# Kernel optimization log

Hardware: AMD Instinct MI355X
Metric: run time of the kernel (lower is better)

Reference implementation:

```python
import jax, jax.numpy as jnp
import numpy as np

N = 50000      # nodes
E = 200000     # edges
IN = 768       # in_dim
HID = 256      # hidden_dim
OUT = 64       # out_dim
H = 4          # heads in conv1
R = 6          # n_relations
NEG = 0.2      # LeakyReLU negative slope (PyG default)
EPS = 1e-5     # LayerNorm eps


def layer_norm(h, g, b):
    mu = jnp.mean(h, axis=-1, keepdims=True)
    var = jnp.mean((h - mu) ** 2, axis=-1, keepdims=True)
    return (h - mu) * jax.lax.rsqrt(var + EPS) * g + b


def gat_layer(x, src, dst, W, a_src, a_dst, bias, heads, dh):
    # project: [N, heads, dh]
    h = (x @ W).reshape(-1, heads, dh)
    # per-node attention logits [N, heads]
    al_s = jnp.sum(h * a_src, axis=-1)
    al_d = jnp.sum(h * a_dst, axis=-1)
    # per-edge scores (edge j->i: source contributes al_s[j], target al_d[i])
    e = jax.nn.leaky_relu(al_s[src] + al_d[dst], NEG)  # [E, heads]
    # segment softmax over edges sharing the same destination node
    e_max = jax.ops.segment_max(e, dst, num_segments=N)        # [N, heads]
    ex = jnp.exp(e - e_max[dst])                               # [E, heads]
    denom = jax.ops.segment_sum(ex, dst, num_segments=N)       # [N, heads]
    alpha = ex / denom[dst]                                    # [E, heads]
    # weighted scatter-aggregate of source messages
    msg = h[src] * alpha[:, :, None]                            # [E, heads, dh]
    out = jax.ops.segment_sum(msg, dst, num_segments=N)        # [N, heads, dh]
    return out.reshape(-1, heads * dh) + bias


def setup_inputs() -> dict:
    key = jax.random.key(0)
    ks = jax.random.split(key, 16)
    s = 0.05  # keep attention logits tame
    return {
        "x": jax.random.normal(ks[0], (N, IN), jnp.float32),
        "edge_index": jax.random.randint(ks[1], (2, E), 0, N, dtype=jnp.int64),
        "edge_type": jax.random.randint(ks[2], (E,), 0, R, dtype=jnp.int64),
        "edge_emb": jax.random.normal(ks[3], (R, IN), jnp.float32) * s,
        "W1": jax.random.normal(ks[4], (IN, H * (HID // H)), jnp.float32) * s,
        "a_src1": jax.random.normal(ks[5], (H, HID // H), jnp.float32) * s,
        "a_dst1": jax.random.normal(ks[6], (H, HID // H), jnp.float32) * s,
        "b1": jnp.zeros((HID,), jnp.float32),
        "g1": jnp.ones((HID,), jnp.float32),
        "be1": jnp.zeros((HID,), jnp.float32),
        "W2": jax.random.normal(ks[7], (HID, OUT), jnp.float32) * s,
        "a_src2": jax.random.normal(ks[8], (1, OUT), jnp.float32) * s,
        "a_dst2": jax.random.normal(ks[9], (1, OUT), jnp.float32) * s,
        "b2": jnp.zeros((OUT,), jnp.float32),
        "g2": jnp.ones((OUT,), jnp.float32),
        "be2": jnp.zeros((OUT,), jnp.float32),
    }


def reference(x, edge_index, edge_type, edge_emb, W1, a_src1, a_dst1, b1, g1, be1,
              W2, a_src2, a_dst2, b2, g2, be2):
    src, dst = edge_index[0], edge_index[1]
    edge_feat = edge_emb[edge_type]                 # [E, IN]
    x_mod = x.at[src].set(x[src] + edge_feat)
    h = gat_layer(x_mod, src, dst, W1, a_src1, a_dst1, b1, H, HID // H)
    h = layer_norm(h, g1, be1)
    h = jax.nn.elu(h)                                # dropout off (inference)
    h = gat_layer(h, src, dst, W2, a_src2, a_dst2, b2, 1, OUT)
    h = layer_norm(h, g2, be2)
    return h
```

## Files before the change

### kernel.cpp

```cpp
#include <hip/hip_runtime.h>
#include <cstdint>
#include <cstddef>

#define NN 50000
#define NE 200000
#define IND 768
#define HID 256
#define OUTD 64
#define NB 196

typedef __bf16 bf16;
typedef __bf16 bf16x8 __attribute__((ext_vector_type(8)));
typedef float f32x4 __attribute__((ext_vector_type(4)));

__device__ __forceinline__ void ld_lds16(const void* g, void* l) {
  __builtin_amdgcn_global_load_lds((const __attribute__((address_space(1))) void*)g,
                                   (__attribute__((address_space(3))) void*)l, 16, 0, 0);
}

__global__ __launch_bounds__(256) void k_edge_prep(const int* __restrict__ ei,
                                                   int* __restrict__ le, int* __restrict__ deg) {
  int e = blockIdx.x * 256 + threadIdx.x;
  if (e < NE) {
    atomicMax(&le[ei[e]], e);
    atomicAdd(&deg[ei[NE + e]], 1);
  }
}

__global__ __launch_bounds__(256) void k_scan_block(const int* __restrict__ deg,
                                                    int* __restrict__ excl, int* __restrict__ bsum) {
  __shared__ int sm[256];
  int tid = threadIdx.x;
  int i = blockIdx.x * 256 + tid;
  int v = (i < NN) ? deg[i] : 0;
  sm[tid] = v;
  __syncthreads();
#pragma unroll
  for (int off = 1; off < 256; off <<= 1) {
    int t = (tid >= off) ? sm[tid - off] : 0;
    __syncthreads();
    sm[tid] += t;
    __syncthreads();
  }
  if (i < NN) excl[i] = sm[tid] - v;
  if (tid == 255) bsum[blockIdx.x] = sm[255];
}

__global__ __launch_bounds__(256) void k_scan_partials(const int* __restrict__ bsum,
                                                       int* __restrict__ bbase) {
  __shared__ int sm[256];
  int tid = threadIdx.x;
  int v = (tid < NB) ? bsum[tid] : 0;
  sm[tid] = v;
  __syncthreads();
#pragma unroll
  for (int off = 1; off < 256; off <<= 1) {
    int t = (tid >= off) ? sm[tid - off] : 0;
    __syncthreads();
    sm[tid] += t;
    __syncthreads();
  }
  bbase[tid] = sm[tid] - v;
}

__global__ __launch_bounds__(256) void k_add_base(const int* __restrict__ excl,
                                                  const int* __restrict__ bbase,
                                                  const int* __restrict__ le,
                                                  const int* __restrict__ et,
                                                  int* __restrict__ rowstart, int* __restrict__ cur,
                                                  int* __restrict__ tmod) {
  int i = blockIdx.x * 256 + threadIdx.x;
  if (i < NN) {
    int rs = excl[i] + bbase[i >> 8];
    rowstart[i] = rs;
    cur[i] = rs;
    int l = le[i];
    tmod[i] = (l >= 0) ? et[l] : -1;
  }
}

__global__ __launch_bounds__(256) void k_scatter_csr(const int* __restrict__ ei,
                                                     int* __restrict__ cur, int* __restrict__ csr) {
  int e = blockIdx.x * 256 + threadIdx.x;
  if (e < NE) {
    int d = ei[NE + e];
    int pos = atomicAdd(&cur[d], 1);
    csr[pos] = ei[e];
  }
}

__global__ __launch_bounds__(256) void k_prep(const float* __restrict__ W1,
                                              const float* __restrict__ W2,
                                              const float* __restrict__ eemb,
                                              bf16* __restrict__ W1t,
                                              bf16* __restrict__ W2t,
                                              float* __restrict__ P) {
  int b = blockIdx.x, tid = threadIdx.x;
  if (b < 768) {
    int k = b, n = tid;
    W1t[n * 768 + k] = (bf16)W1[k * 256 + n];
  } else if (b < 768 + 64) {
    int k = (b - 768) * 4 + (tid >> 6);
    int n = tid & 63;
    W2t[n * 256 + k] = (bf16)W2[k * 64 + n];
  } else {
    int r = b - 832, c = tid;
    float s = 0.f;
    for (int k = 0; k < 768; k++) s += eemb[r * 768 + k] * W1[k * 256 + c];
    P[r * 256 + c] = s;
  }
}

__global__ __launch_bounds__(256) void k_gemm1(const float* __restrict__ Ax,
                                               const bf16* __restrict__ Bt,
                                               const int* __restrict__ tmod,
                                               const float* __restrict__ P,
                                               bf16* __restrict__ C,
                                               const float* __restrict__ aS,
                                               const float* __restrict__ aD,
                                               float* __restrict__ alS,
                                               float* __restrict__ alD) {
  __shared__ float As[128 * 32];
  __shared__ bf16 Bs[128 * 32];
  const int tid = threadIdx.x, lane = tid & 63, wave = tid >> 6;
  const int wr = wave >> 1, wc = wave & 1;
  const int ln15 = lane & 15, q = lane >> 4;
  const int n0 = blockIdx.x * 128, m0 = blockIdx.y * 128;

  const int a_lrow = lane >> 3, a_gch = (lane & 7) ^ a_lrow;
  const int b_lrow = lane >> 2, b_gch = (lane & 3) ^ ((b_lrow >> 1) & 3);

  f32x4 acc[4][4] = {};

  for (int kt = 0; kt < IND; kt += 32) {
    __syncthreads();
#pragma unroll
    for (int j = 0; j < 4; j++) {
      int g = wave * 4 + j;
      int grow = min(m0 + g * 8 + a_lrow, NN - 1);
      ld_lds16(Ax + (size_t)grow * IND + kt + a_gch * 4, As + g * 256);
    }
#pragma unroll
    for (int j = 0; j < 2; j++) {
      int h = wave * 2 + j;
      int grow = h * 16 + b_lrow;
      ld_lds16(Bt + (size_t)(n0 + grow) * IND + kt + b_gch * 8, Bs + h * 512);
    }
    __syncthreads();

    bf16x8 af[4], bfr[4];
    const float4* Asv = (const float4*)As;
#pragma unroll
    for (int mi = 0; mi < 4; mi++) {
      int R = wr * 64 + mi * 16 + ln15, msk = R & 7;
      float4 f0 = Asv[R * 8 + ((2 * q) ^ msk)];
      float4 f1 = Asv[R * 8 + ((2 * q + 1) ^ msk)];
      bf16x8 t;
      t[0] = (bf16)f0.x; t[1] = (bf16)f0.y; t[2] = (bf16)f0.z; t[3] = (bf16)f0.w;
      t[4] = (bf16)f1.x; t[5] = (bf16)f1.y; t[6] = (bf16)f1.z; t[7] = (bf16)f1.w;
      af[mi] = t;
    }
#pragma unroll
    for (int ni = 0; ni < 4; ni++) {
      int R = wc * 64 + ni * 16 + ln15;
      int c = q ^ ((R >> 1) & 3);
      bfr[ni] = *(const bf16x8*)(Bs + R * 32 + c * 8);
    }
#pragma unroll
    for (int mi = 0; mi < 4; mi++)
#pragma unroll
      for (int ni = 0; ni < 4; ni++)
        acc[mi][ni] = __builtin_amdgcn_mfma_f32_16x16x32_bf16(af[mi], bfr[ni], acc[mi][ni], 0, 0, 0);
  }

  const int hd = (n0 + wc * 64) >> 6;
#pragma unroll
  for (int mi = 0; mi < 4; mi++) {
#pragma unroll
    for (int r = 0; r < 4; r++) {
      int row = m0 + wr * 64 + mi * 16 + q * 4 + r;
      bool vr = row < NN;
      int t = tmod[vr ? row : NN - 1];
      float ps = 0.f, pd = 0.f;
#pragma unroll
      for (int ni = 0; ni < 4; ni++) {
        int col = n0 + wc * 64 + ni * 16 + ln15;
        float val = acc[mi][ni][r];
        if (t >= 0) val += P[t * HID + col];
        ps += val * aS[col];
        pd += val * aD[col];
        if (vr) C[(size_t)row * HID + col] = (bf16)val;
      }
#pragma unroll
      for (int o = 1; o < 16; o <<= 1) { ps += __shfl_xor(ps, o); pd += __shfl_xor(pd, o); }
      if (ln15 == 0 && vr) { alS[row * 4 + hd] = ps; alD[row * 4 + hd] = pd; }
    }
  }
}

__global__ __launch_bounds__(256) void k_gemm2(const bf16* __restrict__ A,
                                               const bf16* __restrict__ Bt,
                                               float* __restrict__ C,
                                               const float* __restrict__ aS,
                                               const float* __restrict__ aD,
                                               float* __restrict__ alS,
                                               float* __restrict__ alD) {
  __shared__ bf16 As[128 * 32];
  __shared__ bf16 Bs[64 * 32];
  const int tid = threadIdx.x, lane = tid & 63, wave = tid >> 6;
  const int ln15 = lane & 15, q = lane >> 4;
  const int m0 = blockIdx.x * 128;
  const int b_lrow = lane >> 2, b_gch = (lane & 3) ^ ((b_lrow >> 1) & 3);

  f32x4 acc[2][4] = {};

  for (int kt = 0; kt < HID; kt += 32) {
    __syncthreads();
#pragma unroll
    for (int j = 0; j < 2; j++) {
      int h = wave * 2 + j;
      int grow = min(m0 + h * 16 + b_lrow, NN - 1);
      ld_lds16(A + (size_t)grow * HID + kt + b_gch * 8, As + h * 512);
    }
    {
      int grow = wave * 16 + b_lrow;
      ld_lds16(Bt + (size_t)grow * HID + kt + b_gch * 8, Bs + wave * 512);
    }
    __syncthreads();

    bf16x8 af[2], bfr[4];
#pragma unroll
    for (int mi = 0; mi < 2; mi++) {
      int R = wave * 32 + mi * 16 + ln15;
      int c = q ^ ((R >> 1) & 3);
      af[mi] = *(const bf16x8*)(As + R * 32 + c * 8);
    }
#pragma unroll
    for (int ni = 0; ni < 4; ni++) {
      int R = ni * 16 + ln15;
      int c = q ^ ((R >> 1) & 3);
      bfr[ni] = *(const bf16x8*)(Bs + R * 32 + c * 8);
    }
#pragma unroll
    for (int mi = 0; mi < 2; mi++)
#pragma unroll
      for (int ni = 0; ni < 4; ni++)
        acc[mi][ni] = __builtin_amdgcn_mfma_f32_16x16x32_bf16(af[mi], bfr[ni], acc[mi][ni], 0, 0, 0);
  }

#pragma unroll
  for (int mi = 0; mi < 2; mi++) {
#pragma unroll
    for (int r = 0; r < 4; r++) {
      int row = m0 + wave * 32 + mi * 16 + q * 4 + r;
      bool vr = row < NN;
      float ps = 0.f, pd = 0.f;
#pragma unroll
      for (int ni = 0; ni < 4; ni++) {
        int col = ni * 16 + ln15;
        float val = acc[mi][ni][r];
        ps += val * aS[col];
        pd += val * aD[col];
        if (vr) C[(size_t)row * OUTD + col] = val;
      }
#pragma unroll
      for (int o = 1; o < 16; o <<= 1) { ps += __shfl_xor(ps, o); pd += __shfl_xor(pd, o); }
      if (ln15 == 0 && vr) { alS[row] = ps; alD[row] = pd; }
    }
  }
}

__global__ __launch_bounds__(256) void k_agg_ln1(const int* __restrict__ rowstart,
                                                 const int* __restrict__ deg,
                                                 const int* __restrict__ csr,
                                                 const bf16* __restrict__ h1,
                                                 const float* __restrict__ alS,
                                                 const float* __restrict__ alD,
                                                 const float* __restrict__ b1,
                                                 const float* __restrict__ g1,
                                                 const float* __restrict__ be1,
                                                 bf16* __restrict__ hln) {
  __shared__ float red[8];
  int n = blockIdx.x, f = threadIdx.x, hd = f >> 6;
  int start = rowstart[n], cnt = deg[n];
  float ald = alD[n * 4 + hd];
  float accv = 0.f, accw = 0.f;
  for (int j0 = 0; j0 < cnt; j0 += 8) {
    int m = cnt - j0; m = m > 8 ? 8 : m;
    int sj[8]; float wv[8];
#pragma unroll
    for (int jj = 0; jj < 8; jj++) sj[jj] = (jj < m) ? csr[start + j0 + jj] : 0;
#pragma unroll
    for (int jj = 0; jj < 8; jj++) {
      float lg = alS[sj[jj] * 4 + hd] + ald;
      lg = lg >= 0.f ? lg : 0.2f * lg;
      wv[jj] = (jj < m) ? __expf(lg) : 0.f;
    }
#pragma unroll
    for (int jj = 0; jj < 8; jj++) {
      accv += wv[jj] * (float)h1[(size_t)sj[jj] * HID + f];
      accw += wv[jj];
    }
  }
  float v = (cnt > 0) ? accv / accw : 0.f;
  v += b1[f];
  float s = v, ss = v * v;
#pragma unroll
  for (int off = 32; off; off >>= 1) { s += __shfl_xor(s, off); ss += __shfl_xor(ss, off); }
  if ((f & 63) == 0) { red[f >> 6] = s; red[4 + (f >> 6)] = ss; }
  __syncthreads();
  float tot = red[0] + red[1] + red[2] + red[3];
  float tss = red[4] + red[5] + red[6] + red[7];
  float mu = tot * (1.f / HID);
  float var = tss * (1.f / HID) - mu * mu;
  float y = (v - mu) * rsqrtf(var + 1e-5f) * g1[f] + be1[f];
  y = y > 0.f ? y : __expf(y) - 1.f;
  hln[(size_t)n * HID + f] = (bf16)y;
}

__global__ __launch_bounds__(256) void k_agg_ln2(const int* __restrict__ rowstart,
                                                 const int* __restrict__ deg,
                                                 const int* __restrict__ csr,
                                                 const float* __restrict__ h2,
                                                 const float* __restrict__ alS,
                                                 const float* __restrict__ alD,
                                                 const float* __restrict__ b2,
                                                 const float* __restrict__ g2,
                                                 const float* __restrict__ be2,
                                                 float* __restrict__ out) {
  int n = blockIdx.x * 4 + (threadIdx.x >> 6);
  int f = threadIdx.x & 63;
  int start = rowstart[n], cnt = deg[n];
  float ald = alD[n];
  float accv = 0.f, accw = 0.f;
  for (int j0 = 0; j0 < cnt; j0 += 8) {
    int m = cnt - j0; m = m > 8 ? 8 : m;
    int sj[8]; float wv[8];
#pragma unroll
    for (int jj = 0; jj < 8; jj++) sj[jj] = (jj < m) ? csr[start + j0 + jj] : 0;
#pragma unroll
    for (int jj = 0; jj < 8; jj++) {
      float lg = alS[sj[jj]] + ald;
      lg = lg >= 0.f ? lg : 0.2f * lg;
      wv[jj] = (jj < m) ? __expf(lg) : 0.f;
    }
#pragma unroll
    for (int jj = 0; jj < 8; jj++) {
      accv += wv[jj] * h2[(size_t)sj[jj] * OUTD + f];
      accw += wv[jj];
    }
  }
  float v = (cnt > 0) ? accv / accw : 0.f;
  v += b2[f];
  float s = v, ss = v * v;
#pragma unroll
  for (int off = 32; off; off >>= 1) { s += __shfl_xor(s, off); ss += __shfl_xor(ss, off); }
  float mu = s * (1.f / OUTD);
  float var = ss * (1.f / OUTD) - mu * mu;
  out[(size_t)n * OUTD + f] = (v - mu) * rsqrtf(var + 1e-5f) * g2[f] + be2[f];
}

extern "C" void kernel_launch(void* const* d_in, const int* in_sizes, int n_in,
                              void* d_out, int out_size, void* d_ws, size_t ws_size,
                              hipStream_t stream) {
  const float* x    = (const float*)d_in[0];
  const int*   ei   = (const int*)d_in[1];
  const int*   et   = (const int*)d_in[2];
  const float* eemb = (const float*)d_in[3];
  const float* W1   = (const float*)d_in[4];
  const float* as1  = (const float*)d_in[5];
  const float* ad1  = (const float*)d_in[6];
  const float* b1   = (const float*)d_in[7];
  const float* g1   = (const float*)d_in[8];
  const float* be1  = (const float*)d_in[9];
  const float* W2   = (const float*)d_in[10];
  const float* as2  = (const float*)d_in[11];
  const float* ad2  = (const float*)d_in[12];
  const float* b2   = (const float*)d_in[13];
  const float* g2   = (const float*)d_in[14];
  const float* be2  = (const float*)d_in[15];
  float* out = (float*)d_out;

  char* base = (char*)d_ws;
  size_t off = 0;
  auto alloc = [&](size_t bytes) -> void* {
    void* p = base + off;
    off = (off + bytes + 255) & ~(size_t)255;
    return p;
  };
  int*   le    = (int*)alloc((size_t)NN * 4);
  int*   deg   = (int*)alloc((size_t)NN * 4);
  int*   excl  = (int*)alloc((size_t)NN * 4);
  int*   bsum  = (int*)alloc(256 * 4);
  int*   bbase = (int*)alloc(256 * 4);
  int*   rowst = (int*)alloc((size_t)NN * 4);
  int*   cur   = (int*)alloc((size_t)NN * 4);
  int*   tmod  = (int*)alloc((size_t)NN * 4);
  int*   csr   = (int*)alloc((size_t)NE * 4);
  bf16*  h1    = (bf16*)alloc((size_t)NN * HID * 2);
  float* alS1  = (float*)alloc((size_t)NN * 4 * 4);
  float* alD1  = (float*)alloc((size_t)NN * 4 * 4);
  bf16*  hln   = (bf16*)alloc((size_t)NN * HID * 2);
  float* h2    = (float*)alloc((size_t)NN * OUTD * 4);
  float* alS2  = (float*)alloc((size_t)NN * 4);
  float* alD2  = (float*)alloc((size_t)NN * 4);
  bf16*  W1t   = (bf16*)alloc((size_t)HID * IND * 2);
  bf16*  W2t   = (bf16*)alloc((size_t)OUTD * HID * 2);
  float* P     = (float*)alloc(6 * HID * 4);

  hipMemsetAsync(le, 0xFF, (size_t)NN * 4, stream);
  hipMemsetAsync(deg, 0, (size_t)NN * 4, stream);

  k_edge_prep<<<(NE + 255) / 256, 256, 0, stream>>>(ei, le, deg);
  k_scan_block<<<NB, 256, 0, stream>>>(deg, excl, bsum);
  k_scan_partials<<<1, 256, 0, stream>>>(bsum, bbase);
  k_add_base<<<NB, 256, 0, stream>>>(excl, bbase, le, et, rowst, cur, tmod);
  k_scatter_csr<<<(NE + 255) / 256, 256, 0, stream>>>(ei, cur, csr);

  k_prep<<<838, 256, 0, stream>>>(W1, W2, eemb, W1t, W2t, P);

  k_gemm1<<<dim3(2, (NN + 127) / 128), 256, 0, stream>>>(x, W1t, tmod, P, h1, as1, ad1, alS1, alD1);
  k_agg_ln1<<<NN, 256, 0, stream>>>(rowst, deg, csr, h1, alS1, alD1, b1, g1, be1, hln);

  k_gemm2<<<(NN + 127) / 128, 256, 0, stream>>>(hln, W2t, h2, as2, ad2, alS2, alD2);
  k_agg_ln2<<<NN / 4, 256, 0, stream>>>(rowst, deg, csr, h2, alS2, alD2, b2, g2, be2, out);
}
```

Before: 518.4 us.

## Double-buffer GEMM tiles via registers and simplify aggregation loops

Both GEMM kernels move from direct global-to-LDS async loads with a single buffer to register-staged double buffering. The next K tile is prefetched into registers while MFMAs run on the current LDS buffer, which removes one barrier per iteration. GEMM1 now converts the fp32 A operand to bf16 before the LDS store, halving A's LDS footprint, and XOR swizzles are replaced by 40-element padded rows. The aggregation kernels drop the batched 8-wide gather for a simple per-edge loop, which loses memory-level parallelism on the gathers.

```diff
diff --git a/kernel.cpp b/kernel.cpp
--- a/kernel.cpp
+++ b/kernel.cpp
@@ -10,13 +10,9 @@
 #define NB 196
 
 typedef __bf16 bf16;
+typedef __bf16 bf16x4 __attribute__((ext_vector_type(4)));
 typedef __bf16 bf16x8 __attribute__((ext_vector_type(8)));
 typedef float f32x4 __attribute__((ext_vector_type(4)));
-
-__device__ __forceinline__ void ld_lds16(const void* g, void* l) {
-  __builtin_amdgcn_global_load_lds((const __attribute__((address_space(1))) void*)g,
-                                   (__attribute__((address_space(3))) void*)l, 16, 0, 0);
-}
 
 __global__ __launch_bounds__(256) void k_edge_prep(const int* __restrict__ ei,
                                                    int* __restrict__ le, int* __restrict__ deg) {
@@ -120,57 +116,64 @@
                                                const float* __restrict__ aD,
                                                float* __restrict__ alS,
                                                float* __restrict__ alD) {
-  __shared__ float As[128 * 32];
-  __shared__ bf16 Bs[128 * 32];
+  __shared__ bf16 As[2][128 * 40];
+  __shared__ bf16 Bs[2][128 * 40];
   const int tid = threadIdx.x, lane = tid & 63, wave = tid >> 6;
   const int wr = wave >> 1, wc = wave & 1;
   const int ln15 = lane & 15, q = lane >> 4;
   const int n0 = blockIdx.x * 128, m0 = blockIdx.y * 128;
 
-  const int a_lrow = lane >> 3, a_gch = (lane & 7) ^ a_lrow;
-  const int b_lrow = lane >> 2, b_gch = (lane & 3) ^ ((b_lrow >> 1) & 3);
+  const int ar = tid >> 3, ac = (tid & 7) * 4;
+  const int br = tid >> 2, bc = (tid & 3) * 8;
+
+  int arow[4];
+#pragma unroll
+  for (int j = 0; j < 4; j++) arow[j] = min(m0 + j * 32 + ar, NN - 1);
+
+  float4 rA[4];
+  int4 rB[2];
+  auto loadT = [&](int kt) {
+#pragma unroll
+    for (int j = 0; j < 4; j++)
+      rA[j] = *(const float4*)(Ax + (size_t)arow[j] * IND + kt + ac);
+#pragma unroll
+    for (int j = 0; j < 2; j++)
+      rB[j] = *(const int4*)(Bt + (size_t)(n0 + j * 64 + br) * IND + kt + bc);
+  };
+  auto storeT = [&](int p) {
+#pragma unroll
+    for (int j = 0; j < 4; j++) {
+      bf16x4 t;
+      t[0] = (bf16)rA[j].x; t[1] = (bf16)rA[j].y; t[2] = (bf16)rA[j].z; t[3] = (bf16)rA[j].w;
+      *(bf16x4*)(&As[p][(j * 32 + ar) * 40 + ac]) = t;
+    }
+#pragma unroll
+    for (int j = 0; j < 2; j++)
+      *(int4*)(&Bs[p][(j * 64 + br) * 40 + bc]) = rB[j];
+  };
 
   f32x4 acc[4][4] = {};
-
+  loadT(0);
+  storeT(0);
+  int p = 0;
   for (int kt = 0; kt < IND; kt += 32) {
     __syncthreads();
-#pragma unroll
-    for (int j = 0; j < 4; j++) {
-      int g = wave * 4 + j;
-      int grow = min(m0 + g * 8 + a_lrow, NN - 1);
-      ld_lds16(Ax + (size_t)grow * IND + kt + a_gch * 4, As + g * 256);
-    }
-#pragma unroll
-    for (int j = 0; j < 2; j++) {
-      int h = wave * 2 + j;
-      int grow = h * 16 + b_lrow;
-      ld_lds16(Bt + (size_t)(n0 + grow) * IND + kt + b_gch * 8, Bs + h * 512);
-    }
-    __syncthreads();
-
+    bool more = (kt + 32) < IND;
+    if (more) loadT(kt + 32);
     bf16x8 af[4], bfr[4];
-    const float4* Asv = (const float4*)As;
-#pragma unroll
-    for (int mi = 0; mi < 4; mi++) {
-      int R = wr * 64 + mi * 16 + ln15, msk = R & 7;
-      float4 f0 = Asv[R * 8 + ((2 * q) ^ msk)];
-      float4 f1 = Asv[R * 8 + ((2 * q + 1) ^ msk)];
-      bf16x8 t;
-      t[0] = (bf16)f0.x; t[1] = (bf16)f0.y; t[2] = (bf16)f0.z; t[3] = (bf16)f0.w;
-      t[4] = (bf16)f1.x; t[5] = (bf16)f1.y; t[6] = (bf16)f1.z; t[7] = (bf16)f1.w;
-      af[mi] = t;
-    }
-#pragma unroll
-    for (int ni = 0; ni < 4; ni++) {
-      int R = wc * 64 + ni * 16 + ln15;
-      int c = q ^ ((R >> 1) & 3);
-      bfr[ni] = *(const bf16x8*)(Bs + R * 32 + c * 8);
-    }
+#pragma unroll
+    for (int mi = 0; mi < 4; mi++)
+      af[mi] = *(const bf16x8*)(&As[p][(wr * 64 + mi * 16 + ln15) * 40 + q * 8]);
+#pragma unroll
+    for (int ni = 0; ni < 4; ni++)
+      bfr[ni] = *(const bf16x8*)(&Bs[p][(wc * 64 + ni * 16 + ln15) * 40 + q * 8]);
 #pragma unroll
     for (int mi = 0; mi < 4; mi++)
 #pragma unroll
       for (int ni = 0; ni < 4; ni++)
         acc[mi][ni] = __builtin_amdgcn_mfma_f32_16x16x32_bf16(af[mi], bfr[ni], acc[mi][ni], 0, 0, 0);
+    if (more) storeT(p ^ 1);
+    p ^= 1;
   }
 
   const int hd = (n0 + wc * 64) >> 6;
@@ -205,47 +208,53 @@
                                                const float* __restrict__ aD,
                                                float* __restrict__ alS,
                                                float* __restrict__ alD) {
-  __shared__ bf16 As[128 * 32];
-  __shared__ bf16 Bs[64 * 32];
+  __shared__ bf16 As[2][128 * 40];
+  __shared__ bf16 Bs[2][64 * 40];
   const int tid = threadIdx.x, lane = tid & 63, wave = tid >> 6;
   const int ln15 = lane & 15, q = lane >> 4;
   const int m0 = blockIdx.x * 128;
-  const int b_lrow = lane >> 2, b_gch = (lane & 3) ^ ((b_lrow >> 1) & 3);
+  const int br = tid >> 2, bc = (tid & 3) * 8;
+
+  int arow[2];
+#pragma unroll
+  for (int j = 0; j < 2; j++) arow[j] = min(m0 + j * 64 + br, NN - 1);
+
+  int4 rA[2], rB;
+  auto loadT = [&](int kt) {
+#pragma unroll
+    for (int j = 0; j < 2; j++)
+      rA[j] = *(const int4*)(A + (size_t)arow[j] * HID + kt + bc);
+    rB = *(const int4*)(Bt + (size_t)br * HID + kt + bc);
+  };
+  auto storeT = [&](int p) {
+#pragma unroll
+    for (int j = 0; j < 2; j++)
+      *(int4*)(&As[p][(j * 64 + br) * 40 + bc]) = rA[j];
+    *(int4*)(&Bs[p][br * 40 + bc]) = rB;
+  };
 
   f32x4 acc[2][4] = {};
-
+  loadT(0);
+  storeT(0);
+  int p = 0;
   for (int kt = 0; kt < HID; kt += 32) {
     __syncthreads();
-#pragma unroll
-    for (int j = 0; j < 2; j++) {
-      int h = wave * 2 + j;
-      int grow = min(m0 + h * 16 + b_lrow, NN - 1);
-      ld_lds16(A + (size_t)grow * HID + kt + b_gch * 8, As + h * 512);
-    }
-    {
-      int grow = wave * 16 + b_lrow;
-      ld_lds16(Bt + (size_t)grow * HID + kt + b_gch * 8, Bs + wave * 512);
-    }
-    __syncthreads();
-
+    bool more = (kt + 32) < HID;
+    if (more) loadT(kt + 32);
     bf16x8 af[2], bfr[4];
 #pragma unroll
-    for (int mi = 0; mi < 2; mi++) {
-      int R = wave * 32 + mi * 16 + ln15;
-      int c = q ^ ((R >> 1) & 3);
-      af[mi] = *(const bf16x8*)(As + R * 32 + c * 8);
-    }
-#pragma unroll
-    for (int ni = 0; ni < 4; ni++) {
-      int R = ni * 16 + ln15;
-      int c = q ^ ((R >> 1) & 3);
-      bfr[ni] = *(const bf16x8*)(Bs + R * 32 + c * 8);
-    }
+    for (int mi = 0; mi < 2; mi++)
+      af[mi] = *(const bf16x8*)(&As[p][(wave * 32 + mi * 16 + ln15) * 40 + q * 8]);
+#pragma unroll
+    for (int ni = 0; ni < 4; ni++)
+      bfr[ni] = *(const bf16x8*)(&Bs[p][(ni * 16 + ln15) * 40 + q * 8]);
 #pragma unroll
     for (int mi = 0; mi < 2; mi++)
 #pragma unroll
       for (int ni = 0; ni < 4; ni++)
         acc[mi][ni] = __builtin_amdgcn_mfma_f32_16x16x32_bf16(af[mi], bfr[ni], acc[mi][ni], 0, 0, 0);
+    if (more) storeT(p ^ 1);
+    p ^= 1;
   }
 
 #pragma unroll
@@ -285,22 +294,13 @@
   int start = rowstart[n], cnt = deg[n];
   float ald = alD[n * 4 + hd];
   float accv = 0.f, accw = 0.f;
-  for (int j0 = 0; j0 < cnt; j0 += 8) {
-    int m = cnt - j0; m = m > 8 ? 8 : m;
-    int sj[8]; float wv[8];
-#pragma unroll
-    for (int jj = 0; jj < 8; jj++) sj[jj] = (jj < m) ? csr[start + j0 + jj] : 0;
-#pragma unroll
-    for (int jj = 0; jj < 8; jj++) {
-      float lg = alS[sj[jj] * 4 + hd] + ald;
-      lg = lg >= 0.f ? lg : 0.2f * lg;
-      wv[jj] = (jj < m) ? __expf(lg) : 0.f;
-    }
-#pragma unroll
-    for (int jj = 0; jj < 8; jj++) {
-      accv += wv[jj] * (float)h1[(size_t)sj[jj] * HID + f];
-      accw += wv[jj];
-    }
+  for (int j = 0; j < cnt; j++) {
+    int s = csr[start + j];
+    float lg = alS[s * 4 + hd] + ald;
+    lg = lg >= 0.f ? lg : 0.2f * lg;
+    float w = __expf(lg);
+    accv += w * (float)h1[(size_t)s * HID + f];
+    accw += w;
   }
   float v = (cnt > 0) ? accv / accw : 0.f;
   v += b1[f];
@@ -333,22 +333,13 @@
   int start = rowstart[n], cnt = deg[n];
   float ald = alD[n];
   float accv = 0.f, accw = 0.f;
-  for (int j0 = 0; j0 < cnt; j0 += 8) {
-    int m = cnt - j0; m = m > 8 ? 8 : m;
-    int sj[8]; float wv[8];
-#pragma unroll
-    for (int jj = 0; jj < 8; jj++) sj[jj] = (jj < m) ? csr[start + j0 + jj] : 0;
-#pragma unroll
-    for (int jj = 0; jj < 8; jj++) {
-      float lg = alS[sj[jj]] + ald;
-      lg = lg >= 0.f ? lg : 0.2f * lg;
-      wv[jj] = (jj < m) ? __expf(lg) : 0.f;
-    }
-#pragma unroll
-    for (int jj = 0; jj < 8; jj++) {
-      accv += wv[jj] * h2[(size_t)sj[jj] * OUTD + f];
-      accw += wv[jj];
-    }
+  for (int j = 0; j < cnt; j++) {
+    int s = csr[start + j];
+    float lg = alS[s] + ald;
+    lg = lg >= 0.f ? lg : 0.2f * lg;
+    float w = __expf(lg);
+    accv += w * h2[(size_t)s * OUTD + f];
+    accw += w;
   }
   float v = (cnt > 0) ? accv / accw : 0.f;
   v += b2[f];
```

After: 547.8 us. +5.7%, slower.
